# Kernel tuning notes

Hardware: AMD Instinct MI355X
Metric: run time of the kernel (lower is better)

Reference implementation:

```python
import jax, jax.numpy as jnp
import numpy as np
import math

B, N, E = 1024, 256, 2048
EMBED, H = 39, 64
RATIO = 0.8


def _gcn(x, src, dst, emask, W, b):
    # GCNConv with self-loops and symmetric normalization.
    # x: [n, f_in], src/dst: [E] int, emask: [E] float (0 = pruned edge)
    h = x @ W                                            # [n, f_out]
    deg = jnp.ones(x.shape[0], x.dtype).at[dst].add(emask)  # +1 self loop
    dinv = jax.lax.rsqrt(deg)
    coef = dinv[src] * dinv[dst] * emask                 # [E]
    agg = jnp.zeros_like(h).at[dst].add(h[src] * coef[:, None])
    return agg + h / deg[:, None] + b                    # self-loop norm = 1/deg


def _topk(x, src, dst, emask, p, k):
    # PyG TopKPooling: score = tanh(x.p/||p||); keep top-k nodes; gate x by score;
    # edges with a dropped endpoint are masked out (static-shape equivalent of filtering).
    score = jnp.tanh((x @ p) / jnp.linalg.norm(p))       # [n]
    vals, idx = jax.lax.top_k(score, k)                  # [k]
    xn = x[idx] * vals[:, None]                          # gated node features
    newid = jnp.full((x.shape[0],), -1, dtype=src.dtype).at[idx].set(
        jnp.arange(k, dtype=src.dtype))
    ns, nd = newid[src], newid[dst]
    valid = emask * ((ns >= 0) & (nd >= 0)).astype(emask.dtype)
    return xn, jnp.maximum(ns, 0), jnp.maximum(nd, 0), valid


def _readout(x):
    # global max pool || global mean pool over nodes of one graph
    return jnp.concatenate([jnp.max(x, axis=0), jnp.mean(x, axis=0)], axis=0)


def _graph_forward(x, src, dst, W1, b1, p1, W2, b2, p2, W3, b3, p3):
    emask = jnp.ones(src.shape, x.dtype)
    n = N
    x = jax.nn.relu(_gcn(x, src, dst, emask, W1, b1))
    k1 = math.ceil(RATIO * n)
    x, src, dst, emask = _topk(x, src, dst, emask, p1, k1)
    r1 = _readout(x)
    x = jax.nn.relu(_gcn(x, src, dst, emask, W2, b2))
    k2 = math.ceil(RATIO * k1)
    x, src, dst, emask = _topk(x, src, dst, emask, p2, k2)
    r2 = _readout(x)
    x = jax.nn.relu(_gcn(x, src, dst, emask, W3, b3))
    k3 = math.ceil(RATIO * k2)
    x, src, dst, emask = _topk(x, src, dst, emask, p3, k3)
    r3 = _readout(x)
    return r1 + r2 + r3                                  # [128]


def setup_inputs() -> dict:
    key = jax.random.key(0)
    ks = jax.random.split(key, 16)
    s = 0.1
    inp = {
        'x': jax.random.normal(ks[0], (B, N, EMBED), jnp.float32),
        'edge_index': jax.random.randint(ks[1], (B, 2, E), 0, N, jnp.int64),
        'W1': jax.random.normal(ks[2], (EMBED, H), jnp.float32) * s,
        'b1': jnp.zeros((H,), jnp.float32),
        'p1': jax.random.normal(ks[3], (H,), jnp.float32),
        'W2': jax.random.normal(ks[4], (H, H), jnp.float32) * s,
        'b2': jnp.zeros((H,), jnp.float32),
        'p2': jax.random.normal(ks[5], (H,), jnp.float32),
        'W3': jax.random.normal(ks[6], (H, H), jnp.float32) * s,
        'b3': jnp.zeros((H,), jnp.float32),
        'p3': jax.random.normal(ks[7], (H,), jnp.float32),
        'lW1': jax.random.normal(ks[8], (2 * H, 64), jnp.float32) * s,
        'lb1': jnp.zeros((64,), jnp.float32),
        'lW2': jax.random.normal(ks[9], (64, 32), jnp.float32) * s,
        'lb2': jnp.zeros((32,), jnp.float32),
        'lW3': jax.random.normal(ks[10], (32, 1), jnp.float32) * s,
        'lb3': jnp.zeros((1,), jnp.float32),
    }
    return inp


def reference(x, edge_index, W1, b1, p1, W2, b2, p2, W3, b3, p3,
              lW1, lb1, lW2, lb2, lW3, lb3):
    src, dst = edge_index[:, 0, :], edge_index[:, 1, :]
    feats = jax.vmap(_graph_forward,
                     in_axes=(0, 0, 0) + (None,) * 9)(
        x, src, dst, W1, b1, p1, W2, b2, p2, W3, b3, p3)  # [B, 128]
    h = jax.nn.relu(feats @ lW1 + lb1)
    h = jax.nn.relu(h @ lW2 + lb2)
    # dropout is identity in eval mode
    return jax.nn.sigmoid(h @ lW3 + lb3)[:, 0]            # [B]
```

## Files before the change

kernel.cpp:

```cpp
#include <hip/hip_runtime.h>
#include <math.h>

#define NGRAPH 1024
#define NN     256
#define NE     2048
#define EMB    39
#define HD     64
#define NT     512
#define K1 205
#define K2 164
#define K3 132

#define SMEM_BYTES 77456

struct Lds {
    float* feat; float* red; unsigned short* epk;
    float* partial; unsigned char* col; int* ipart;
    int* cnt; int* cur; float* dinv; float* score;
    float* feats; float* pn; float* mlp1; float* mlp2; short* nodemap;
};

__device__ __forceinline__ int fswz(int row, int k) {
    return row * 64 + (((((k >> 2)) ^ (row & 7)) << 2) | (k & 3));
}

template<int FIN>
__device__ __forceinline__ void layer_body(
    const Lds& S, const int* __restrict__ eb,
    const float* __restrict__ W, const float* __restrict__ bvec,
    const float* __restrict__ pvec, int n, int kkeep, int tid)
{
    const int node = tid & 255;
    const int q    = tid >> 8;
    const int joU  = __builtin_amdgcn_readfirstlane(q * 32);
    const int jb0  = q * 8;
    const int lane = tid & 63;
    const bool active = node < n;

    if (tid < 258) S.cnt[tid] = 0;
    if (tid < 64) {
        float pv = pvec[tid];
        float s2 = pv * pv;
        #pragma unroll
        for (int off = 32; off >= 1; off >>= 1) s2 += __shfl_xor(s2, off, 64);
        S.pn[tid] = pv * rsqrtf(s2);
    }
    __syncthreads();

    {
        const int4* src4 = (const int4*)eb;
        const int4* dst4 = (const int4*)(eb + NE);
        int4 sv = src4[tid];
        int4 dv = dst4[tid];
        int ss[4] = { S.nodemap[sv.x], S.nodemap[sv.y], S.nodemap[sv.z], S.nodemap[sv.w] };
        int dd[4] = { S.nodemap[dv.x], S.nodemap[dv.y], S.nodemap[dv.z], S.nodemap[dv.w] };
        unsigned short pk[4];
        #pragma unroll
        for (int t = 0; t < 4; t++) {
            int s = ss[t], d = dd[t];
            pk[t] = 0xFFFFu;
            if ((s | d) >= 0) {
                pk[t] = (unsigned short)(s | (d << 8));
                atomicAdd(&S.cnt[d], 1);
            }
        }
        *(ushort4*)(S.epk + tid * 4) = make_ushort4(pk[0], pk[1], pk[2], pk[3]);
    }
    __syncthreads();

    if (tid < 64) {
        int base = tid * 4;
        int4 c = *(const int4*)(S.cnt + base);
        int s4 = c.x + c.y + c.z + c.w;
        int x = s4;
        #pragma unroll
        for (int off = 1; off < 64; off <<= 1) {
            int t = __shfl_up(x, off, 64);
            if (tid >= off) x += t;
        }
        int e0 = x - s4;
        int4 off4 = make_int4(e0, e0 + c.x, e0 + c.x + c.y, e0 + c.x + c.y + c.z);
        *(int4*)(S.cnt + base) = off4;
        *(int4*)(S.cur + base) = off4;
        *(float4*)(S.dinv + base) = make_float4(
            rsqrtf((float)(1 + c.x)), rsqrtf((float)(1 + c.y)),
            rsqrtf((float)(1 + c.z)), rsqrtf((float)(1 + c.w)));
        if (tid == 63) S.cnt[256] = x;
    }
    __syncthreads();

    {
        ushort4 pk4 = *(const ushort4*)(S.epk + tid * 4);
        unsigned short pks[4] = { pk4.x, pk4.y, pk4.z, pk4.w };
        #pragma unroll
        for (int t = 0; t < 4; t++) {
            unsigned pk = pks[t];
            if (pk != 0xFFFFu) {
                int d = pk >> 8;
                int pos = atomicAdd(&S.cur[d], 1);
                S.col[pos] = (unsigned char)(pk & 0xFFu);
            }
        }
    }
    float h[32];
    if (active) {
        #pragma unroll
        for (int j = 0; j < 32; j++) h[j] = 0.f;
        const float* Wp   = W + joU;
        const float* xrow = S.feat + node * 64;
        const int rs = node & 7;
        if (FIN == EMB) {
            #pragma unroll
            for (int u = 0; u < 9; u++) {
                float4 xv = *(const float4*)(xrow + ((u ^ rs) << 2));
                float xs[4] = { xv.x, xv.y, xv.z, xv.w };
                #pragma unroll
                for (int t = 0; t < 4; t++) {
                    int k = u * 4 + t;
                    #pragma unroll
                    for (int j = 0; j < 32; j++) h[j] = fmaf(xs[t], Wp[k * HD + j], h[j]);
                }
            }
            #pragma unroll
            for (int k = 36; k < 39; k++) {
                float xv = xrow[((9 ^ rs) << 2) + (k - 36)];
                #pragma unroll
                for (int j = 0; j < 32; j++) h[j] = fmaf(xv, Wp[k * HD + j], h[j]);
            }
        } else {
            #pragma unroll 4
            for (int u = 0; u < 16; u++) {
                float4 xv = *(const float4*)(xrow + ((u ^ rs) << 2));
                float xs[4] = { xv.x, xv.y, xv.z, xv.w };
                #pragma unroll
                for (int t = 0; t < 4; t++) {
                    int k = u * 4 + t;
                    #pragma unroll
                    for (int j = 0; j < 32; j++) h[j] = fmaf(xs[t], Wp[k * HD + j], h[j]);
                }
            }
        }
    }
    __syncthreads();

    if (active) {
        const int rs = node & 7;
        #pragma unroll
        for (int u = 0; u < 8; u++) {
            float4 v;
            v.x = h[u * 4 + 0]; v.y = h[u * 4 + 1]; v.z = h[u * 4 + 2]; v.w = h[u * 4 + 3];
            *(float4*)(S.feat + node * 64 + (((jb0 + u) ^ rs) << 2)) = v;
        }
    }
    __syncthreads();

    float s1[32];
    float sc = 0.f;
    if (active) {
        int o0 = S.cnt[node], o1 = S.cnt[node + 1];
        #pragma unroll
        for (int j = 0; j < 32; j++) s1[j] = 0.f;
        if (o0 < o1) {
            int sN = S.col[o0];
            for (int e = o0; e < o1; e++) {
                int s = sN;
                int en = (e + 1 < o1) ? (e + 1) : e;
                sN = S.col[en];
                float dv = S.dinv[s];
                const float* hs = S.feat + s * 64;
                const int ssz = s & 7;
                #pragma unroll
                for (int u = 0; u < 8; u++) {
                    float4 hv = *(const float4*)(hs + (((jb0 + u) ^ ssz) << 2));
                    s1[u * 4 + 0] = fmaf(dv, hv.x, s1[u * 4 + 0]);
                    s1[u * 4 + 1] = fmaf(dv, hv.y, s1[u * 4 + 1]);
                    s1[u * 4 + 2] = fmaf(dv, hv.z, s1[u * 4 + 2]);
                    s1[u * 4 + 3] = fmaf(dv, hv.w, s1[u * 4 + 3]);
                }
            }
        }
        float dvd = S.dinv[node];
        float invdeg = dvd * dvd;
        const float* bU   = bvec + joU;
        const float* hown = S.feat + node * 64;
        const int rs = node & 7;
        #pragma unroll
        for (int u = 0; u < 8; u++) {
            float4 hv = *(const float4*)(hown + (((jb0 + u) ^ rs) << 2));
            float hs[4] = { hv.x, hv.y, hv.z, hv.w };
            #pragma unroll
            for (int t = 0; t < 4; t++) {
                int j = u * 4 + t;
                float o = fmaf(dvd, s1[j], fmaf(hs[t], invdeg, bU[j]));
                o = fmaxf(o, 0.f);
                s1[j] = o;
                sc = fmaf(o, S.pn[joU + j], sc);
            }
        }
    }
    __syncthreads();

    S.partial[tid] = sc;
    __syncthreads();

    if (tid < 256) S.score[tid] = tanhf(S.partial[tid] + S.partial[tid + 256]);
    __syncthreads();

    {
        int j0 = joU * 4;
        int j1 = (j0 + 128 < n) ? (j0 + 128) : n;
        float si = S.score[node];
        int c = 0;
        int j = j0;
        for (; j + 4 <= j1; j += 4) {
            float4 s4 = *(const float4*)&S.score[j];
            c += (s4.x > si) || (s4.x == si && (j + 0) < node);
            c += (s4.y > si) || (s4.y == si && (j + 1) < node);
            c += (s4.z > si) || (s4.z == si && (j + 2) < node);
            c += (s4.w > si) || (s4.w == si && (j + 3) < node);
        }
        for (; j < j1; j++) {
            float sj = S.score[j];
            c += (sj > si) || (sj == si && j < node);
        }
        S.ipart[tid] = c;
    }
    __syncthreads();

    if (tid < 256) S.cur[tid] = S.ipart[tid] + S.ipart[tid + 256];
    __syncthreads();

    if (tid < 256) {
        int m = S.nodemap[tid];
        if (m >= 0) {
            int r = S.cur[m];
            S.nodemap[tid] = (short)((r < kkeep) ? r : -1);
        }
    }
    if (active) {
        int r = S.cur[node];
        if (r < kkeep) {
            float v = S.score[node];
            const int rr = r & 7;
            #pragma unroll
            for (int u = 0; u < 8; u++) {
                float4 w4;
                w4.x = s1[u * 4 + 0] * v; w4.y = s1[u * 4 + 1] * v;
                w4.z = s1[u * 4 + 2] * v; w4.w = s1[u * 4 + 3] * v;
                *(float4*)(S.feat + r * 64 + (((jb0 + u) ^ rr) << 2)) = w4;
            }
        }
    }
    __syncthreads();

    {
        int w = tid >> 6;
        float mx = -3.4e38f, sm = 0.f;
        for (int rr = w; rr < kkeep; rr += 8) {
            float v = S.feat[rr * 64 + ((((lane >> 2) ^ (rr & 7)) << 2) | (lane & 3))];
            mx = fmaxf(mx, v);
            sm += v;
        }
        S.red[w * 64 + lane]       = mx;
        S.red[512 + w * 64 + lane] = sm;
    }
    __syncthreads();

    if (tid < 64) {
        float mx = S.red[tid], sm = S.red[512 + tid];
        #pragma unroll
        for (int w = 1; w < 8; w++) {
            mx = fmaxf(mx, S.red[w * 64 + tid]);
            sm += S.red[512 + w * 64 + tid];
        }
        S.feats[tid]      += mx;
        S.feats[64 + tid] += sm / (float)kkeep;
    }
    __syncthreads();
}

__global__ __launch_bounds__(NT, 4) void gnn_pool_kernel(
    const float* __restrict__ gx, const int* __restrict__ gedge,
    const float* __restrict__ W1, const float* __restrict__ b1, const float* __restrict__ p1,
    const float* __restrict__ W2, const float* __restrict__ b2, const float* __restrict__ p2,
    const float* __restrict__ W3, const float* __restrict__ b3, const float* __restrict__ p3,
    const float* __restrict__ lW1, const float* __restrict__ lb1,
    const float* __restrict__ lW2, const float* __restrict__ lb2,
    const float* __restrict__ lW3, const float* __restrict__ lb3,
    float* __restrict__ gout)
{
    extern __shared__ __align__(16) char smem_raw[];
    Lds S;
    S.feat    = (float*)smem_raw;
    S.red     = S.feat + NN * 64;
    S.epk     = (unsigned short*)S.red;
    S.partial = S.red + 1024;
    S.col     = (unsigned char*)S.partial;
    S.ipart   = (int*)S.partial;
    S.cnt     = (int*)(S.partial + 512);
    S.cur     = S.cnt + 260;
    S.dinv    = (float*)(S.cur + 256);
    S.score   = S.dinv + 256;
    S.feats   = S.score + 256;
    S.pn      = S.feats + 128;
    S.mlp1    = S.pn + 64;
    S.mlp2    = S.mlp1 + 64;
    S.nodemap = (short*)(S.mlp2 + 32);

    const int tid = threadIdx.x;
    const int b   = blockIdx.x;
    const int* eb = gedge + (size_t)b * 2 * NE;

    {
        const float4* xb4 = (const float4*)(gx + (size_t)b * NN * EMB);
        for (int i = tid; i < (NN * EMB) / 4; i += NT) {
            float4 v = xb4[i];
            int g = i * 4;
            float vs[4] = { v.x, v.y, v.z, v.w };
            #pragma unroll
            for (int t = 0; t < 4; t++) {
                int gg = g + t;
                int nd = gg / EMB;
                int k  = gg - nd * EMB;
                S.feat[fswz(nd, k)] = vs[t];
            }
        }
        if (tid < NN) S.nodemap[tid] = (short)tid;
        if (tid < 2 * HD) S.feats[tid] = 0.f;
    }
    __syncthreads();

    layer_body<EMB>(S, eb, W1, b1, p1, NN, K1, tid);
    layer_body<HD >(S, eb, W2, b2, p2, K1, K2, tid);
    layer_body<HD >(S, eb, W3, b3, p3, K2, K3, tid);

    if (tid < 64) {
        float a = lb1[tid];
        for (int i = 0; i < 2 * HD; i++) a = fmaf(S.feats[i], lW1[i * 64 + tid], a);
        S.mlp1[tid] = fmaxf(a, 0.f);
    }
    __syncthreads();
    if (tid < 32) {
        float a = lb2[tid];
        for (int i = 0; i < 64; i++) a = fmaf(S.mlp1[i], lW2[i * 32 + tid], a);
        S.mlp2[tid] = fmaxf(a, 0.f);
    }
    __syncthreads();
    if (tid == 0) {
        float a = lb3[0];
        for (int i = 0; i < 32; i++) a = fmaf(S.mlp2[i], lW3[i], a);
        gout[b] = 1.0f / (1.0f + expf(-a));
    }
}

extern "C" void kernel_launch(void* const* d_in, const int* in_sizes, int n_in,
                              void* d_out, int out_size, void* d_ws, size_t ws_size,
                              hipStream_t stream) {
    const float* gx    = (const float*)d_in[0];
    const int*   gedge = (const int*)d_in[1];
    const float* W1 = (const float*)d_in[2];
    const float* b1 = (const float*)d_in[3];
    const float* p1 = (const float*)d_in[4];
    const float* W2 = (const float*)d_in[5];
    const float* b2 = (const float*)d_in[6];
    const float* p2 = (const float*)d_in[7];
    const float* W3 = (const float*)d_in[8];
    const float* b3 = (const float*)d_in[9];
    const float* p3 = (const float*)d_in[10];
    const float* lW1 = (const float*)d_in[11];
    const float* lb1 = (const float*)d_in[12];
    const float* lW2 = (const float*)d_in[13];
    const float* lb2 = (const float*)d_in[14];
    const float* lW3 = (const float*)d_in[15];
    const float* lb3 = (const float*)d_in[16];
    float* gout = (float*)d_out;

    (void)hipFuncSetAttribute((const void*)gnn_pool_kernel,
                              hipFuncAttributeMaxDynamicSharedMemorySize, SMEM_BYTES);

    gnn_pool_kernel<<<NGRAPH, NT, SMEM_BYTES, stream>>>(
        gx, gedge, W1, b1, p1, W2, b2, p2, W3, b3, p3,
        lW1, lb1, lW2, lb2, lW3, lb3, gout);
}
```

Baseline: 268.3 us.

## Double block size to 1024 threads, splitting feature columns four ways

Raises the per-graph workgroup from 512 to 1024 threads, so each thread handles 16 output features instead of 32 and 2 edges instead of 4. Partial score and rank sums now reduce over four slices, and shared-memory regions are rearranged so partial/ipart alias the red buffer and col gets its own space. The aim is more parallelism and lower register pressure per thread, at the cost of more synchronisation participants, idle waves in the readout phase, and possibly fewer resident blocks per CU.

Result: no change. 270.1 us (+0.7%).

```diff
diff --git a/kernel.cpp b/kernel.cpp
--- a/kernel.cpp
+++ b/kernel.cpp
@@ -6,7 +6,7 @@
 #define NE     2048
 #define EMB    39
 #define HD     64
-#define NT     512
+#define NT     1024
 #define K1 205
 #define K2 164
 #define K3 132
@@ -14,8 +14,9 @@
 #define SMEM_BYTES 77456
 
 struct Lds {
-    float* feat; float* red; unsigned short* epk;
-    float* partial; unsigned char* col; int* ipart;
+    float* feat;
+    float* red; unsigned short* epk; float* partial; int* ipart;
+    unsigned char* col;
     int* cnt; int* cur; float* dinv; float* score;
     float* feats; float* pn; float* mlp1; float* mlp2; short* nodemap;
 };
@@ -32,8 +33,8 @@
 {
     const int node = tid & 255;
     const int q    = tid >> 8;
-    const int joU  = __builtin_amdgcn_readfirstlane(q * 32);
-    const int jb0  = q * 8;
+    const int joU  = __builtin_amdgcn_readfirstlane(q * 16);
+    const int jb0  = q * 4;
     const int lane = tid & 63;
     const bool active = node < n;
 
@@ -48,15 +49,13 @@
     __syncthreads();
 
     {
-        const int4* src4 = (const int4*)eb;
-        const int4* dst4 = (const int4*)(eb + NE);
-        int4 sv = src4[tid];
-        int4 dv = dst4[tid];
-        int ss[4] = { S.nodemap[sv.x], S.nodemap[sv.y], S.nodemap[sv.z], S.nodemap[sv.w] };
-        int dd[4] = { S.nodemap[dv.x], S.nodemap[dv.y], S.nodemap[dv.z], S.nodemap[dv.w] };
-        unsigned short pk[4];
-        #pragma unroll
-        for (int t = 0; t < 4; t++) {
+        int2 sv = ((const int2*)eb)[tid];
+        int2 dv = ((const int2*)(eb + NE))[tid];
+        int ss[2] = { S.nodemap[sv.x], S.nodemap[sv.y] };
+        int dd[2] = { S.nodemap[dv.x], S.nodemap[dv.y] };
+        unsigned short pk[2];
+        #pragma unroll
+        for (int t = 0; t < 2; t++) {
             int s = ss[t], d = dd[t];
             pk[t] = 0xFFFFu;
             if ((s | d) >= 0) {
@@ -64,7 +63,7 @@
                 atomicAdd(&S.cnt[d], 1);
             }
         }
-        *(ushort4*)(S.epk + tid * 4) = make_ushort4(pk[0], pk[1], pk[2], pk[3]);
+        *(ushort2*)(S.epk + tid * 2) = make_ushort2(pk[0], pk[1]);
     }
     __syncthreads();
 
@@ -90,10 +89,10 @@
     __syncthreads();
 
     {
-        ushort4 pk4 = *(const ushort4*)(S.epk + tid * 4);
-        unsigned short pks[4] = { pk4.x, pk4.y, pk4.z, pk4.w };
-        #pragma unroll
-        for (int t = 0; t < 4; t++) {
+        ushort2 pk2 = *(const ushort2*)(S.epk + tid * 2);
+        unsigned short pks[2] = { pk2.x, pk2.y };
+        #pragma unroll
+        for (int t = 0; t < 2; t++) {
             unsigned pk = pks[t];
             if (pk != 0xFFFFu) {
                 int d = pk >> 8;
@@ -102,10 +101,10 @@
             }
         }
     }
-    float h[32];
+    float h[16];
     if (active) {
         #pragma unroll
-        for (int j = 0; j < 32; j++) h[j] = 0.f;
+        for (int j = 0; j < 16; j++) h[j] = 0.f;
         const float* Wp   = W + joU;
         const float* xrow = S.feat + node * 64;
         const int rs = node & 7;
@@ -118,14 +117,14 @@
                 for (int t = 0; t < 4; t++) {
                     int k = u * 4 + t;
                     #pragma unroll
-                    for (int j = 0; j < 32; j++) h[j] = fmaf(xs[t], Wp[k * HD + j], h[j]);
+                    for (int j = 0; j < 16; j++) h[j] = fmaf(xs[t], Wp[k * HD + j], h[j]);
                 }
             }
             #pragma unroll
             for (int k = 36; k < 39; k++) {
                 float xv = xrow[((9 ^ rs) << 2) + (k - 36)];
                 #pragma unroll
-                for (int j = 0; j < 32; j++) h[j] = fmaf(xv, Wp[k * HD + j], h[j]);
+                for (int j = 0; j < 16; j++) h[j] = fmaf(xv, Wp[k * HD + j], h[j]);
             }
         } else {
             #pragma unroll 4
@@ -136,7 +135,7 @@
                 for (int t = 0; t < 4; t++) {
                     int k = u * 4 + t;
                     #pragma unroll
-                    for (int j = 0; j < 32; j++) h[j] = fmaf(xs[t], Wp[k * HD + j], h[j]);
+                    for (int j = 0; j < 16; j++) h[j] = fmaf(xs[t], Wp[k * HD + j], h[j]);
                 }
             }
         }
@@ -146,7 +145,7 @@
     if (active) {
         const int rs = node & 7;
         #pragma unroll
-        for (int u = 0; u < 8; u++) {
+        for (int u = 0; u < 4; u++) {
             float4 v;
             v.x = h[u * 4 + 0]; v.y = h[u * 4 + 1]; v.z = h[u * 4 + 2]; v.w = h[u * 4 + 3];
             *(float4*)(S.feat + node * 64 + (((jb0 + u) ^ rs) << 2)) = v;
@@ -154,12 +153,12 @@
     }
     __syncthreads();
 
-    float s1[32];
+    float s1[16];
     float sc = 0.f;
     if (active) {
         int o0 = S.cnt[node], o1 = S.cnt[node + 1];
         #pragma unroll
-        for (int j = 0; j < 32; j++) s1[j] = 0.f;
+        for (int j = 0; j < 16; j++) s1[j] = 0.f;
         if (o0 < o1) {
             int sN = S.col[o0];
             for (int e = o0; e < o1; e++) {
@@ -170,7 +169,7 @@
                 const float* hs = S.feat + s * 64;
                 const int ssz = s & 7;
                 #pragma unroll
-                for (int u = 0; u < 8; u++) {
+                for (int u = 0; u < 4; u++) {
                     float4 hv = *(const float4*)(hs + (((jb0 + u) ^ ssz) << 2));
                     s1[u * 4 + 0] = fmaf(dv, hv.x, s1[u * 4 + 0]);
                     s1[u * 4 + 1] = fmaf(dv, hv.y, s1[u * 4 + 1]);
@@ -185,7 +184,7 @@
         const float* hown = S.feat + node * 64;
         const int rs = node & 7;
         #pragma unroll
-        for (int u = 0; u < 8; u++) {
+        for (int u = 0; u < 4; u++) {
             float4 hv = *(const float4*)(hown + (((jb0 + u) ^ rs) << 2));
             float hs[4] = { hv.x, hv.y, hv.z, hv.w };
             #pragma unroll
@@ -203,12 +202,14 @@
     S.partial[tid] = sc;
     __syncthreads();
 
-    if (tid < 256) S.score[tid] = tanhf(S.partial[tid] + S.partial[tid + 256]);
+    if (tid < 256)
+        S.score[tid] = tanhf(S.partial[tid] + S.partial[tid + 256] +
+                             S.partial[tid + 512] + S.partial[tid + 768]);
     __syncthreads();
 
     {
         int j0 = joU * 4;
-        int j1 = (j0 + 128 < n) ? (j0 + 128) : n;
+        int j1 = (j0 + 64 < n) ? (j0 + 64) : n;
         float si = S.score[node];
         int c = 0;
         int j = j0;
@@ -227,7 +228,9 @@
     }
     __syncthreads();
 
-    if (tid < 256) S.cur[tid] = S.ipart[tid] + S.ipart[tid + 256];
+    if (tid < 256)
+        S.cur[tid] = S.ipart[tid] + S.ipart[tid + 256] +
+                     S.ipart[tid + 512] + S.ipart[tid + 768];
     __syncthreads();
 
     if (tid < 256) {
@@ -243,7 +246,7 @@
             float v = S.score[node];
             const int rr = r & 7;
             #pragma unroll
-            for (int u = 0; u < 8; u++) {
+            for (int u = 0; u < 4; u++) {
                 float4 w4;
                 w4.x = s1[u * 4 + 0] * v; w4.y = s1[u * 4 + 1] * v;
                 w4.z = s1[u * 4 + 2] * v; w4.w = s1[u * 4 + 3] * v;
@@ -255,14 +258,16 @@
 
     {
         int w = tid >> 6;
-        float mx = -3.4e38f, sm = 0.f;
-        for (int rr = w; rr < kkeep; rr += 8) {
-            float v = S.feat[rr * 64 + ((((lane >> 2) ^ (rr & 7)) << 2) | (lane & 3))];
-            mx = fmaxf(mx, v);
-            sm += v;
-        }
-        S.red[w * 64 + lane]       = mx;
-        S.red[512 + w * 64 + lane] = sm;
+        if (w < 8) {
+            float mx = -3.4e38f, sm = 0.f;
+            for (int rr = w; rr < kkeep; rr += 8) {
+                float v = S.feat[rr * 64 + ((((lane >> 2) ^ (rr & 7)) << 2) | (lane & 3))];
+                mx = fmaxf(mx, v);
+                sm += v;
+            }
+            S.red[w * 64 + lane]       = mx;
+            S.red[512 + w * 64 + lane] = sm;
+        }
     }
     __syncthreads();
 
@@ -279,7 +284,7 @@
     __syncthreads();
 }
 
-__global__ __launch_bounds__(NT, 4) void gnn_pool_kernel(
+__global__ __launch_bounds__(NT, 8) void gnn_pool_kernel(
     const float* __restrict__ gx, const int* __restrict__ gedge,
     const float* __restrict__ W1, const float* __restrict__ b1, const float* __restrict__ p1,
     const float* __restrict__ W2, const float* __restrict__ b2, const float* __restrict__ p2,
@@ -294,10 +299,10 @@
     S.feat    = (float*)smem_raw;
     S.red     = S.feat + NN * 64;
     S.epk     = (unsigned short*)S.red;
-    S.partial = S.red + 1024;
-    S.col     = (unsigned char*)S.partial;
-    S.ipart   = (int*)S.partial;
-    S.cnt     = (int*)(S.partial + 512);
+    S.partial = S.red;
+    S.ipart   = (int*)S.red;
+    S.col     = (unsigned char*)(S.red + 1024);
+    S.cnt     = (int*)(S.col + 2048);
     S.cur     = S.cnt + 260;
     S.dinv    = (float*)(S.cur + 256);
     S.score   = S.dinv + 256;
```

## Sort nodes by in-degree so aggregation wavefronts have balanced loop trips

Applied to the files above, without the earlier changes.

Computes each node's in-degree rank through an all-pairs comparison count and builds a permutation (dsort) that assigns nodes to threads in descending degree order. The neighbour aggregation, scoring and ranking phases then index through this permutation, so lanes in a wavefront get similar edge counts and spend fewer iterations diverged. The cost is an extra O(n^2/2)-per-thread degree ranking pass, LDS atomics, indirect indexing and a small increase in shared memory. The LDS layout is reshuffled so that col no longer aliases partial/ipart, since col is now still needed while those buffers are being written.

New measurement: 306.2 us. 1.14x slower.

```diff
diff --git a/kernel.cpp b/kernel.cpp
--- a/kernel.cpp
+++ b/kernel.cpp
@@ -11,13 +11,15 @@
 #define K2 164
 #define K3 132
 
-#define SMEM_BYTES 77456
+#define SMEM_BYTES 78224
 
 struct Lds {
-    float* feat; float* red; unsigned short* epk;
-    float* partial; unsigned char* col; int* ipart;
+    float* feat;
+    float* red; unsigned short* epk; float* partial; int* ipart;
+    unsigned char* col;
     int* cnt; int* cur; float* dinv; float* score;
     float* feats; float* pn; float* mlp1; float* mlp2; short* nodemap;
+    unsigned char* degu8; short* dsort;
 };
 
 __device__ __forceinline__ int fswz(int row, int k) {
@@ -36,14 +38,16 @@
     const int jb0  = q * 8;
     const int lane = tid & 63;
     const bool active = node < n;
+    int* scoreInt = (int*)S.score;
 
     if (tid < 258) S.cnt[tid] = 0;
+    if (tid < 256) scoreInt[tid] = 0;
     if (tid < 64) {
         float pv = pvec[tid];
-        float s2 = pv * pv;
-        #pragma unroll
-        for (int off = 32; off >= 1; off >>= 1) s2 += __shfl_xor(s2, off, 64);
-        S.pn[tid] = pv * rsqrtf(s2);
+        float s2v = pv * pv;
+        #pragma unroll
+        for (int off = 32; off >= 1; off >>= 1) s2v += __shfl_xor(s2v, off, 64);
+        S.pn[tid] = pv * rsqrtf(s2v);
     }
     __syncthreads();
 
@@ -85,10 +89,32 @@
         *(float4*)(S.dinv + base) = make_float4(
             rsqrtf((float)(1 + c.x)), rsqrtf((float)(1 + c.y)),
             rsqrtf((float)(1 + c.z)), rsqrtf((float)(1 + c.w)));
+        unsigned d0 = c.x > 255 ? 255u : (unsigned)c.x;
+        unsigned d1 = c.y > 255 ? 255u : (unsigned)c.y;
+        unsigned d2 = c.z > 255 ? 255u : (unsigned)c.z;
+        unsigned d3 = c.w > 255 ? 255u : (unsigned)c.w;
+        ((unsigned*)S.degu8)[tid] = d0 | (d1 << 8) | (d2 << 16) | (d3 << 24);
         if (tid == 63) S.cnt[256] = x;
     }
     __syncthreads();
 
+    {
+        int dg = S.degu8[node];
+        int j0 = q * 128;
+        const unsigned* dw = (const unsigned*)(S.degu8 + j0);
+        int c = 0;
+        #pragma unroll 8
+        for (int w = 0; w < 32; w++) {
+            unsigned wv = dw[w];
+            int j = j0 + w * 4;
+            #pragma unroll
+            for (int t = 0; t < 4; t++) {
+                int dj = (wv >> (8 * t)) & 255;
+                c += (dj > dg) || (dj == dg && (j + t) < node);
+            }
+        }
+        atomicAdd(&scoreInt[node], c);
+    }
     {
         ushort4 pk4 = *(const ushort4*)(S.epk + tid * 4);
         unsigned short pks[4] = { pk4.x, pk4.y, pk4.z, pk4.w };
@@ -152,12 +178,15 @@
             *(float4*)(S.feat + node * 64 + (((jb0 + u) ^ rs) << 2)) = v;
         }
     }
-    __syncthreads();
-
+    if (tid < 256) S.dsort[scoreInt[tid]] = (short)tid;
+    __syncthreads();
+
+    const int nd = S.dsort[node];
+    const bool act5 = nd < n;
     float s1[32];
     float sc = 0.f;
-    if (active) {
-        int o0 = S.cnt[node], o1 = S.cnt[node + 1];
+    if (act5) {
+        int o0 = S.cnt[nd], o1 = S.cnt[nd + 1];
         #pragma unroll
         for (int j = 0; j < 32; j++) s1[j] = 0.f;
         if (o0 < o1) {
@@ -179,11 +208,11 @@
                 }
             }
         }
-        float dvd = S.dinv[node];
+        float dvd = S.dinv[nd];
         float invdeg = dvd * dvd;
         const float* bU   = bvec + joU;
-        const float* hown = S.feat + node * 64;
-        const int rs = node & 7;
+        const float* hown = S.feat + nd * 64;
+        const int rs = nd & 7;
         #pragma unroll
         for (int u = 0; u < 8; u++) {
             float4 hv = *(const float4*)(hown + (((jb0 + u) ^ rs) << 2));
@@ -203,31 +232,39 @@
     S.partial[tid] = sc;
     __syncthreads();
 
-    if (tid < 256) S.score[tid] = tanhf(S.partial[tid] + S.partial[tid + 256]);
-    __syncthreads();
-
-    {
-        int j0 = joU * 4;
-        int j1 = (j0 + 128 < n) ? (j0 + 128) : n;
-        float si = S.score[node];
+    if (tid < 256) {
+        int nd2 = S.dsort[tid];
+        S.score[nd2] = tanhf(S.partial[tid] + S.partial[tid + 256]);
+    }
+    __syncthreads();
+
+    {
         int c = 0;
-        int j = j0;
-        for (; j + 4 <= j1; j += 4) {
-            float4 s4 = *(const float4*)&S.score[j];
-            c += (s4.x > si) || (s4.x == si && (j + 0) < node);
-            c += (s4.y > si) || (s4.y == si && (j + 1) < node);
-            c += (s4.z > si) || (s4.z == si && (j + 2) < node);
-            c += (s4.w > si) || (s4.w == si && (j + 3) < node);
-        }
-        for (; j < j1; j++) {
-            float sj = S.score[j];
-            c += (sj > si) || (sj == si && j < node);
+        if (act5) {
+            int j0 = joU * 4;
+            int j1 = (j0 + 128 < n) ? (j0 + 128) : n;
+            float si = S.score[nd];
+            int j = j0;
+            for (; j + 4 <= j1; j += 4) {
+                float4 s4 = *(const float4*)&S.score[j];
+                c += (s4.x > si) || (s4.x == si && (j + 0) < nd);
+                c += (s4.y > si) || (s4.y == si && (j + 1) < nd);
+                c += (s4.z > si) || (s4.z == si && (j + 2) < nd);
+                c += (s4.w > si) || (s4.w == si && (j + 3) < nd);
+            }
+            for (; j < j1; j++) {
+                float sj = S.score[j];
+                c += (sj > si) || (sj == si && j < nd);
+            }
         }
         S.ipart[tid] = c;
     }
     __syncthreads();
 
-    if (tid < 256) S.cur[tid] = S.ipart[tid] + S.ipart[tid + 256];
+    if (tid < 256) {
+        int nd2 = S.dsort[tid];
+        S.cur[nd2] = S.ipart[tid] + S.ipart[tid + 256];
+    }
     __syncthreads();
 
     if (tid < 256) {
@@ -237,10 +274,10 @@
             S.nodemap[tid] = (short)((r < kkeep) ? r : -1);
         }
     }
-    if (active) {
-        int r = S.cur[node];
+    if (act5) {
+        int r = S.cur[nd];
         if (r < kkeep) {
-            float v = S.score[node];
+            float v = S.score[nd];
             const int rr = r & 7;
             #pragma unroll
             for (int u = 0; u < 8; u++) {
@@ -294,10 +331,10 @@
     S.feat    = (float*)smem_raw;
     S.red     = S.feat + NN * 64;
     S.epk     = (unsigned short*)S.red;
-    S.partial = S.red + 1024;
-    S.col     = (unsigned char*)S.partial;
-    S.ipart   = (int*)S.partial;
-    S.cnt     = (int*)(S.partial + 512);
+    S.partial = S.red;
+    S.ipart   = (int*)S.red;
+    S.col     = (unsigned char*)(S.red + 1024);
+    S.cnt     = (int*)(S.col + 2048);
     S.cur     = S.cnt + 260;
     S.dinv    = (float*)(S.cur + 256);
     S.score   = S.dinv + 256;
@@ -306,6 +343,8 @@
     S.mlp1    = S.pn + 64;
     S.mlp2    = S.mlp1 + 64;
     S.nodemap = (short*)(S.mlp2 + 32);
+    S.degu8   = (unsigned char*)(S.nodemap + 256);
+    S.dsort   = (short*)(S.degu8 + 256);
 
     const int tid = threadIdx.x;
     const int b   = blockIdx.x;
```
